# Performance work log

Measured on AMD Instinct MI355X. Metric: run time of the kernel, lower is better.

The kernel has to match this reference:

```python
import jax, jax.numpy as jnp
import numpy as np

DIM = 384
HEADS = 12
HD = DIM // HEADS  # 32
WIN = 16
N = WIN * WIN      # 256
B = 256            # num_windows * batch
K = 5              # dwc kernel size
EPS = 1e-6


def setup_inputs() -> dict:
    key = jax.random.key(0)
    ks = jax.random.split(key, 8)
    u = lambda k, shape, fan_in: jax.random.uniform(
        k, shape, jnp.float32, -1.0 / np.sqrt(fan_in), 1.0 / np.sqrt(fan_in))
    return {
        "x": jax.random.normal(ks[0], (B, N, DIM), jnp.float32),
        # nn.Linear(dim, 3*dim): weight [3C, C], bias [3C]
        "qkv_w": u(ks[1], (3 * DIM, DIM), DIM),
        "qkv_b": u(ks[2], (3 * DIM,), DIM),
        # nn.Parameter initialized to zeros
        "pos_enc": jnp.zeros((1, N, DIM), jnp.float32),
        # depthwise Conv2d(HD, HD, K, groups=HD): weight [HD, 1, K, K]
        "dwc_w": u(ks[3], (HD, 1, K, K), K * K),
        "dwc_b": u(ks[4], (HD,), K * K),
        "proj_w": u(ks[5], (DIM, DIM), DIM),
        "proj_b": u(ks[6], (DIM,), DIM),
    }


def reference(x, qkv_w, qkv_b, pos_enc, dwc_w, dwc_b, proj_w, proj_b):
    Bsz, Nn, C = x.shape
    qkv = x @ qkv_w.T + qkv_b                     # [B, N, 3C]
    q, k, v = jnp.split(qkv, 3, axis=-1)          # each [B, N, C]
    k = k + pos_enc
    q = jax.nn.relu(q)
    k = jax.nn.relu(k)

    def to_heads(t):  # 'b n (h c) -> (b h) n c'
        return t.reshape(Bsz, Nn, HEADS, HD).transpose(0, 2, 1, 3).reshape(Bsz * HEADS, Nn, HD)

    q, k, v = to_heads(q), to_heads(k), to_heads(v)
    # explicit fp32 (autocast disabled block in original)
    qf = q.astype(jnp.float32)
    kf = k.astype(jnp.float32)
    vf = v.astype(jnp.float32)

    z = 1.0 / (jnp.einsum('bic,bc->bi', qf, kf.sum(axis=1)) + EPS)  # [BH, N]

    i = j = Nn
    c = d = HD
    if i * j * (c + d) > c * d * (i + j):  # kv-first (true for N=256, HD=32)
        kv = jnp.einsum('bjc,bjd->bcd', kf, vf)            # [BH, c, d]
        out = jnp.einsum('bic,bcd,bi->bid', qf, kv, z)     # [BH, N, d]
    else:
        qk = jnp.einsum('bic,bjc->bij', qf, kf)
        out = jnp.einsum('bij,bjd,bi->bid', qk, vf, z)

    # depthwise conv on v: 'b (w h) c -> b c w h'
    num = int(Nn ** 0.5)
    fm = vf.reshape(Bsz * HEADS, num, num, HD).transpose(0, 3, 1, 2)  # NCHW
    fm = jax.lax.conv_general_dilated(
        fm, dwc_w, window_strides=(1, 1),
        padding=[(K // 2, K // 2), (K // 2, K // 2)],
        dimension_numbers=('NCHW', 'OIHW', 'NCHW'),
        feature_group_count=HD)
    fm = fm + dwc_b[None, :, None, None]
    fm = fm.transpose(0, 2, 3, 1).reshape(Bsz * HEADS, Nn, HD)  # 'b c w h -> b (w h) c'

    out = out + fm
    # '(b h) n c -> b n (h c)'
    out = out.reshape(Bsz, HEADS, Nn, HD).transpose(0, 2, 1, 3).reshape(Bsz, Nn, C)
    return out @ proj_w.T + proj_b
```

## Files before the change

kernel.cpp:

```cpp
#include <hip/hip_runtime.h>
#include <stdint.h>
#include <stddef.h>


typedef _Float16 f16;
typedef __attribute__((ext_vector_type(4))) _Float16 f16x4;
typedef __attribute__((ext_vector_type(8))) _Float16 f16x8;
typedef __attribute__((ext_vector_type(4))) float floatx4;

#define DEV __device__ __forceinline__

DEV void async16(const void* g, void* l) {
  __builtin_amdgcn_global_load_lds(
      (const __attribute__((address_space(1))) void*)g,
      (__attribute__((address_space(3))) void*)l,
      16, 0, 0);
}

DEV floatx4 mfma16(f16x8 a, f16x8 b, floatx4 c) {
  return __builtin_amdgcn_mfma_f32_16x16x32_f16(a, b, c, 0, 0, 0);
}

DEV f16x4 cvt4(float4 v) {
  f16x4 h;
  h[0] = (f16)v.x; h[1] = (f16)v.y; h[2] = (f16)v.z; h[3] = (f16)v.w;
  return h;
}

__global__ __launch_bounds__(256) void cvt_kernel(
    const float* __restrict__ src, f16* __restrict__ dst, int n4) {
  const int stride = gridDim.x * 256;
  for (int i = blockIdx.x * 256 + threadIdx.x; i < n4; i += stride) {
    float4 v = ((const float4*)src)[i];
    ((f16x4*)dst)[i] = cvt4(v);
  }
}

__global__ __launch_bounds__(256) void qkv_kernel(
    const f16* __restrict__ A, const f16* __restrict__ W,
    const float* __restrict__ bias, const float* __restrict__ pos,
    f16* __restrict__ q_ws, f16* __restrict__ kT_ws, f16* __restrict__ vT_ws) {
  __shared__ __align__(16) f16 Af[2][128 * 64];
  __shared__ __align__(16) f16 Wf[2][128 * 64];
  const int tid = threadIdx.x;
  const int lane = tid & 63, wave = tid >> 6;
  const int quad = lane >> 4, lr = lane & 15;
  const int wm = wave >> 1, wn = wave & 1;
  const int bx = blockIdx.x;
  const int ga = bx / 72, rem = bx - ga * 72;
  const int nblk = rem >> 3, gc = rem & 7;
  const int m0 = (ga * 8 + gc) * 128, n0 = nblk * 128;
  const int rl = lane >> 3;
  const int lcol = (lane & 7) ^ rl;

  floatx4 acc[4][4] = {};

  const f16* ap[4];
  const f16* wp[4];
#pragma unroll
  for (int t2 = 0; t2 < 4; ++t2) {
    const int row = (wave * 4 + t2) * 8 + rl;
    ap[t2] = A + (size_t)(m0 + row) * 384 + lcol * 8;
    wp[t2] = W + (size_t)(n0 + row) * 384 + lcol * 8;
  }

#pragma unroll
  for (int t2 = 0; t2 < 4; ++t2) {
    const int ch = wave * 4 + t2;
    async16(ap[t2], (char*)Af[0] + ch * 1024);
    async16(wp[t2], (char*)Wf[0] + ch * 1024);
  }
  __syncthreads();

#pragma unroll
  for (int kt = 0; kt < 6; ++kt) {
    const int p = kt & 1;
    if (kt < 5) {
#pragma unroll
      for (int t2 = 0; t2 < 4; ++t2) {
        const int ch = wave * 4 + t2;
        async16(ap[t2] + (kt + 1) * 64, (char*)Af[p ^ 1] + ch * 1024);
        async16(wp[t2] + (kt + 1) * 64, (char*)Wf[p ^ 1] + ch * 1024);
      }
    }
#pragma unroll
    for (int s = 0; s < 2; ++s) {
      const int pc = ((quad + s * 4) ^ (lr & 7)) * 16;
      f16x8 af[4], wf[4];
#pragma unroll
      for (int mt = 0; mt < 4; ++mt)
        af[mt] = *(const f16x8*)((const char*)Af[p] +
                                 (wm * 64 + mt * 16 + lr) * 128 + pc);
#pragma unroll
      for (int nt = 0; nt < 4; ++nt)
        wf[nt] = *(const f16x8*)((const char*)Wf[p] +
                                 (wn * 64 + nt * 16 + lr) * 128 + pc);
#pragma unroll
      for (int mt = 0; mt < 4; ++mt)
#pragma unroll
        for (int nt = 0; nt < 4; ++nt)
          acc[mt][nt] = mfma16(af[mt], wf[nt], acc[mt][nt]);
    }
    __syncthreads();
  }

  float bv[4];
#pragma unroll
  for (int nt = 0; nt < 4; ++nt)
    bv[nt] = bias[n0 + wn * 64 + nt * 16 + lr];

  const int cls = nblk / 3;
  const int cbase = (nblk - cls * 3) * 128;
  if (cls == 0) {
#pragma unroll
    for (int mt = 0; mt < 4; ++mt) {
#pragma unroll
      for (int r = 0; r < 4; ++r) {
        const int m = m0 + wm * 64 + mt * 16 + quad * 4 + r;
        const int bwin = m >> 8, t = m & 255;
#pragma unroll
        for (int nt = 0; nt < 4; ++nt) {
          const int c = cbase + wn * 64 + nt * 16 + lr;
          const int h = c >> 5, hd = c & 31;
          const float val = fmaxf(acc[mt][nt][r] + bv[nt], 0.f);
          q_ws[(size_t)(bwin * 12 + h) * 8192 + t * 32 + hd] = (f16)val;
        }
      }
    }
  } else {
#pragma unroll
    for (int mt = 0; mt < 4; ++mt) {
      const int mb = m0 + wm * 64 + mt * 16 + quad * 4;
      const int bwin = mb >> 8, t0 = mb & 255;
#pragma unroll
      for (int nt = 0; nt < 4; ++nt) {
        const int c = cbase + wn * 64 + nt * 16 + lr;
        const int h = c >> 5, hd = c & 31;
        f16x4 pk;
        if (cls == 1) {
#pragma unroll
          for (int r = 0; r < 4; ++r)
            pk[r] = (f16)fmaxf(acc[mt][nt][r] + bv[nt] + pos[(t0 + r) * 384 + c], 0.f);
          *(f16x4*)(kT_ws + (size_t)(bwin * 12 + h) * 8192 + hd * 256 + t0) = pk;
        } else {
#pragma unroll
          for (int r = 0; r < 4; ++r)
            pk[r] = (f16)(acc[mt][nt][r] + bv[nt]);
          *(f16x4*)(vT_ws + (size_t)(bwin * 12 + h) * 8192 + hd * 256 + t0) = pk;
        }
      }
    }
  }
}

__global__ __launch_bounds__(256) void attn_kernel(
    const f16* __restrict__ q_ws, const f16* __restrict__ kT_ws,
    const f16* __restrict__ vT_ws, const float* __restrict__ dwc_w,
    const float* __restrict__ dwc_b, f16* __restrict__ y_ws) {
  __shared__ __align__(16) char khb[16640];
  __shared__ __align__(16) char vhb[16640];
  __shared__ float psum[8 * 32];
  __shared__ float ksum[4][32];
  __shared__ float zbuf[256];
  __shared__ __align__(16) f16 kvT[32 * 40];

  const int tid = threadIdx.x;
  const int lane = tid & 63, wave = tid >> 6;
  const int quad = lane >> 4, lr = lane & 15;
  const size_t base = (size_t)blockIdx.x * 8192;

#pragma unroll
  for (int t2 = 0; t2 < 4; ++t2) {
    const int is = wave * 4 + t2;
    async16(kT_ws + base + is * 512 + lane * 8, khb + is * 1040);
    async16(vT_ws + base + is * 512 + lane * 8, vhb + is * 1040);
  }
  __syncthreads();

  {
    const int c = tid & 31, seg = tid >> 5;
    const char* kr = khb + (c >> 1) * 1040 + (c & 1) * 512;
    float s = 0.f;
#pragma unroll
    for (int j8 = 0; j8 < 32; j8 += 8) {
      f16x8 a = *(const f16x8*)(kr + (seg * 32 + j8) * 2);
#pragma unroll
      for (int j = 0; j < 8; ++j) s += (float)a[j];
    }
    psum[seg * 32 + c] = s;
  }
  {
    const int m2 = wave & 1, n2 = wave >> 1;
    const int ck = m2 * 16 + lr, cv = n2 * 16 + lr;
    const char* krow = khb + (ck >> 1) * 1040 + (ck & 1) * 512;
    const char* vrow = vhb + (cv >> 1) * 1040 + (cv & 1) * 512;
    floatx4 kacc = {};
#pragma unroll
    for (int s = 0; s < 8; ++s) {
      f16x8 ka = *(const f16x8*)(krow + (s * 32 + quad * 8) * 2);
      f16x8 vb = *(const f16x8*)(vrow + (s * 32 + quad * 8) * 2);
      kacc = mfma16(ka, vb, kacc);
    }
    f16x4 kk;
#pragma unroll
    for (int r = 0; r < 4; ++r) kk[r] = (f16)kacc[r];
    *(f16x4*)(kvT + (n2 * 16 + lr) * 40 + m2 * 16 + quad * 4) = kk;
  }
  __syncthreads();

  if (lane < 32) {
    float s = 0.f;
#pragma unroll
    for (int seg = 0; seg < 8; ++seg) s += psum[seg * 32 + lane];
    ksum[wave][lane] = s;
  }

  {
    uint32_t* fmu = (uint32_t*)khb;
    const int cg = lr, xr = wave * 4 + quad, c0 = cg * 2;
    float a0[16], a1[16];
    const float b0v = dwc_b[c0], b1v = dwc_b[c0 + 1];
#pragma unroll
    for (int yy = 0; yy < 16; ++yy) { a0[yy] = b0v; a1[yy] = b1v; }
    const char* v0 = vhb + cg * 1040;
#pragma unroll
    for (int dx = 0; dx < 5; ++dx) {
      const int xx = xr + dx - 2;
      if (xx < 0 || xx > 15) continue;
      float r0[16], r1[16];
      f16x8 h0 = *(const f16x8*)(v0 + xx * 32);
      f16x8 h1 = *(const f16x8*)(v0 + xx * 32 + 16);
      f16x8 h2 = *(const f16x8*)(v0 + 512 + xx * 32);
      f16x8 h3 = *(const f16x8*)(v0 + 512 + xx * 32 + 16);
#pragma unroll
      for (int j = 0; j < 8; ++j) {
        r0[j] = (float)h0[j]; r0[8 + j] = (float)h1[j];
        r1[j] = (float)h2[j]; r1[8 + j] = (float)h3[j];
      }
#pragma unroll
      for (int dy = 0; dy < 5; ++dy) {
        const float w0 = dwc_w[c0 * 25 + dx * 5 + dy];
        const float w1 = dwc_w[(c0 + 1) * 25 + dx * 5 + dy];
#pragma unroll
        for (int yy = 0; yy < 16; ++yy) {
          const int ys = yy + dy - 2;
          if (ys >= 0 && ys < 16) {
            a0[yy] += w0 * r0[ys];
            a1[yy] += w1 * r1[ys];
          }
        }
      }
    }
#pragma unroll
    for (int yy = 0; yy < 16; ++yy) {
      const uint32_t lo = (uint32_t)__builtin_bit_cast(uint16_t, (f16)a0[yy]);
      const uint32_t hi = (uint32_t)__builtin_bit_cast(uint16_t, (f16)a1[yy]);
      fmu[(xr * 16 + yy) * 16 + cg] = lo | (hi << 16);
    }
  }

  {
    f16x8 qa[4], kb[2];
#pragma unroll
    for (int mm = 0; mm < 4; ++mm)
      qa[mm] = *(const f16x8*)(q_ws + base +
                               (size_t)(wave * 64 + mm * 16 + lr) * 32 + quad * 8);

    float ksv[8];
#pragma unroll
    for (int j = 0; j < 8; ++j) ksv[j] = ksum[wave][quad * 8 + j];
#pragma unroll
    for (int mm = 0; mm < 4; ++mm) {
      float dot = 0.f;
#pragma unroll
      for (int j = 0; j < 8; ++j) dot += (float)qa[mm][j] * ksv[j];
      dot += __shfl_xor(dot, 16);
      dot += __shfl_xor(dot, 32);
      if (quad == 0) zbuf[wave * 64 + mm * 16 + lr] = 1.f / (dot + 1e-6f);
    }

    floatx4 oacc[4][2] = {};
#pragma unroll
    for (int nt = 0; nt < 2; ++nt)
      kb[nt] = *(const f16x8*)(kvT + (nt * 16 + lr) * 40 + quad * 8);
#pragma unroll
    for (int mm = 0; mm < 4; ++mm)
#pragma unroll
      for (int nt = 0; nt < 2; ++nt)
        oacc[mm][nt] = mfma16(qa[mm], kb[nt], oacc[mm][nt]);

    const f16* fmb = (const f16*)khb;
#pragma unroll
    for (int mm = 0; mm < 4; ++mm) {
#pragma unroll
      for (int r = 0; r < 4; ++r) {
        const int i = wave * 64 + mm * 16 + quad * 4 + r;
        const float zi = zbuf[i];
#pragma unroll
        for (int nt = 0; nt < 2; ++nt) {
          const int d = nt * 16 + lr;
          const float val = oacc[mm][nt][r] * zi + (float)fmb[i * 32 + d];
          y_ws[base + (size_t)i * 32 + d] = (f16)val;
        }
      }
    }
  }
}

__global__ __launch_bounds__(256) void proj_kernel(
    const f16* __restrict__ Y, const f16* __restrict__ Wh,
    const float* __restrict__ bias, float* __restrict__ out) {
  __shared__ __align__(16) f16 Af[2][128 * 64];
  __shared__ __align__(16) f16 Wf[2][128 * 64];
  const int tid = threadIdx.x;
  const int lane = tid & 63, wave = tid >> 6;
  const int quad = lane >> 4, lr = lane & 15;
  const int wm = wave >> 1, wn = wave & 1;
  const int bx = blockIdx.x;
  const int ga = bx / 24, rem = bx - ga * 24;
  const int nblk = rem >> 3, gc = rem & 7;
  const int m0 = (ga * 8 + gc) * 128, n0 = nblk * 128;
  const int bwin = m0 >> 8, tbase = m0 & 255;
  const int rl = lane >> 3;
  const int lcol = (lane & 7) ^ rl;

  floatx4 acc[4][4] = {};

  const f16* ap[4];
  const f16* wp[4];
#pragma unroll
  for (int t2 = 0; t2 < 4; ++t2) {
    const int rowl = (wave * 4 + t2) * 8 + rl;
    ap[t2] = Y + (size_t)(bwin * 12 + (lcol >> 2)) * 8192 +
             (size_t)(tbase + rowl) * 32 + (lcol & 3) * 8;
    wp[t2] = Wh + (size_t)(n0 + rowl) * 384 + lcol * 8;
  }

#pragma unroll
  for (int t2 = 0; t2 < 4; ++t2) {
    const int ch = wave * 4 + t2;
    async16(ap[t2], (char*)Af[0] + ch * 1024);
    async16(wp[t2], (char*)Wf[0] + ch * 1024);
  }
  __syncthreads();

#pragma unroll
  for (int kt = 0; kt < 6; ++kt) {
    const int p = kt & 1;
    if (kt < 5) {
#pragma unroll
      for (int t2 = 0; t2 < 4; ++t2) {
        const int ch = wave * 4 + t2;
        async16(ap[t2] + (size_t)(kt + 1) * 16384, (char*)Af[p ^ 1] + ch * 1024);
        async16(wp[t2] + (kt + 1) * 64, (char*)Wf[p ^ 1] + ch * 1024);
      }
    }
#pragma unroll
    for (int s = 0; s < 2; ++s) {
      const int pc = ((quad + s * 4) ^ (lr & 7)) * 16;
      f16x8 af[4], wf[4];
#pragma unroll
      for (int mt = 0; mt < 4; ++mt)
        af[mt] = *(const f16x8*)((const char*)Af[p] +
                                 (wm * 64 + mt * 16 + lr) * 128 + pc);
#pragma unroll
      for (int nt = 0; nt < 4; ++nt)
        wf[nt] = *(const f16x8*)((const char*)Wf[p] +
                                 (wn * 64 + nt * 16 + lr) * 128 + pc);
#pragma unroll
      for (int mt = 0; mt < 4; ++mt)
#pragma unroll
        for (int nt = 0; nt < 4; ++nt)
          acc[mt][nt] = mfma16(af[mt], wf[nt], acc[mt][nt]);
    }
    __syncthreads();
  }

  float bv[4];
#pragma unroll
  for (int nt = 0; nt < 4; ++nt)
    bv[nt] = bias[n0 + wn * 64 + nt * 16 + lr];
#pragma unroll
  for (int mt = 0; mt < 4; ++mt)
#pragma unroll
    for (int r = 0; r < 4; ++r) {
      const int m = m0 + wm * 64 + mt * 16 + quad * 4 + r;
#pragma unroll
      for (int nt = 0; nt < 4; ++nt) {
        const int n = n0 + wn * 64 + nt * 16 + lr;
        out[(size_t)m * 384 + n] = acc[mt][nt][r] + bv[nt];
      }
    }
}

extern "C" void kernel_launch(void* const* d_in, const int* in_sizes, int n_in,
                              void* d_out, int out_size, void* d_ws, size_t ws_size,
                              hipStream_t stream) {
  const float* x = (const float*)d_in[0];
  const float* qkv_w = (const float*)d_in[1];
  const float* qkv_b = (const float*)d_in[2];
  const float* pos = (const float*)d_in[3];
  const float* dwc_w = (const float*)d_in[4];
  const float* dwc_b = (const float*)d_in[5];
  const float* proj_w = (const float*)d_in[6];
  const float* proj_b = (const float*)d_in[7];
  float* out = (float*)d_out;

  const size_t WS_NEEDED = 150994944;
  if (ws_size < WS_NEEDED) return;

  char* ws = (char*)d_ws;
  f16* q_ws = (f16*)(ws);
  f16* kT_ws = (f16*)(ws + 50331648);
  f16* vT_ws = (f16*)(ws + 100663296);

  f16* xh = (f16*)d_out;
  f16* qwh = (f16*)((char*)d_out + 50331648);
  f16* pwh = (f16*)(ws + 50331648);

  cvt_kernel<<<2048, 256, 0, stream>>>(x, xh, 6291456);
  cvt_kernel<<<432, 256, 0, stream>>>(qkv_w, qwh, 110592);
  qkv_kernel<<<4608, 256, 0, stream>>>(xh, qwh, qkv_b, pos,
                                       q_ws, kT_ws, vT_ws);
  attn_kernel<<<3072, 256, 0, stream>>>(q_ws, kT_ws, vT_ws,
                                        dwc_w, dwc_b, q_ws );
  cvt_kernel<<<144, 256, 0, stream>>>(proj_w, pwh, 36864);
  proj_kernel<<<1536, 256, 0, stream>>>(q_ws, pwh, proj_b, out);
}
```

Measured before the change: 359.7 us.

## Single-buffer QKV GEMM tiles, stage Q epilogue through LDS, prefetch Q early

The QKV GEMM drops LDS double buffering and instead syncs, loads, and computes each k-tile in turn, halving the shared memory it uses. The freed LDS then holds the Q output tile in a swizzled layout, so q_ws is written as contiguous 16-byte vectors instead of scattered 2-byte stores. The attention kernel issues its Q fragment loads before the barrier so they overlap the async K/V loads. The cost is that global-to-LDS transfers no longer overlap with MFMA work inside the GEMM, though higher occupancy may partly hide this.

```diff
diff --git a/kernel.cpp b/kernel.cpp
--- a/kernel.cpp
+++ b/kernel.cpp
@@ -40,8 +40,8 @@
     const f16* __restrict__ A, const f16* __restrict__ W,
     const float* __restrict__ bias, const float* __restrict__ pos,
     f16* __restrict__ q_ws, f16* __restrict__ kT_ws, f16* __restrict__ vT_ws) {
-  __shared__ __align__(16) f16 Af[2][128 * 64];
-  __shared__ __align__(16) f16 Wf[2][128 * 64];
+  __shared__ __align__(16) f16 Af[128 * 64];
+  __shared__ __align__(16) f16 Wf[128 * 64];
   const int tid = threadIdx.x;
   const int lane = tid & 63, wave = tid >> 6;
   const int quad = lane >> 4, lr = lane & 15;
@@ -64,36 +64,26 @@
     wp[t2] = W + (size_t)(n0 + row) * 384 + lcol * 8;
   }
 
-#pragma unroll
-  for (int t2 = 0; t2 < 4; ++t2) {
-    const int ch = wave * 4 + t2;
-    async16(ap[t2], (char*)Af[0] + ch * 1024);
-    async16(wp[t2], (char*)Wf[0] + ch * 1024);
-  }
-  __syncthreads();
-
-#pragma unroll
   for (int kt = 0; kt < 6; ++kt) {
-    const int p = kt & 1;
-    if (kt < 5) {
-#pragma unroll
-      for (int t2 = 0; t2 < 4; ++t2) {
-        const int ch = wave * 4 + t2;
-        async16(ap[t2] + (kt + 1) * 64, (char*)Af[p ^ 1] + ch * 1024);
-        async16(wp[t2] + (kt + 1) * 64, (char*)Wf[p ^ 1] + ch * 1024);
-      }
-    }
+    __syncthreads();
+#pragma unroll
+    for (int t2 = 0; t2 < 4; ++t2) {
+      const int ch = wave * 4 + t2;
+      async16(ap[t2] + kt * 64, (char*)Af + ch * 1024);
+      async16(wp[t2] + kt * 64, (char*)Wf + ch * 1024);
+    }
+    __syncthreads();
 #pragma unroll
     for (int s = 0; s < 2; ++s) {
       const int pc = ((quad + s * 4) ^ (lr & 7)) * 16;
       f16x8 af[4], wf[4];
 #pragma unroll
       for (int mt = 0; mt < 4; ++mt)
-        af[mt] = *(const f16x8*)((const char*)Af[p] +
+        af[mt] = *(const f16x8*)((const char*)Af +
                                  (wm * 64 + mt * 16 + lr) * 128 + pc);
 #pragma unroll
       for (int nt = 0; nt < 4; ++nt)
-        wf[nt] = *(const f16x8*)((const char*)Wf[p] +
+        wf[nt] = *(const f16x8*)((const char*)Wf +
                                  (wn * 64 + nt * 16 + lr) * 128 + pc);
 #pragma unroll
       for (int mt = 0; mt < 4; ++mt)
@@ -101,7 +91,6 @@
         for (int nt = 0; nt < 4; ++nt)
           acc[mt][nt] = mfma16(af[mt], wf[nt], acc[mt][nt]);
     }
-    __syncthreads();
   }
 
   float bv[4];
@@ -112,20 +101,38 @@
   const int cls = nblk / 3;
   const int cbase = (nblk - cls * 3) * 128;
   if (cls == 0) {
+    __syncthreads();
+    f16* buf = wn ? Wf : Af;
 #pragma unroll
     for (int mt = 0; mt < 4; ++mt) {
 #pragma unroll
-      for (int r = 0; r < 4; ++r) {
-        const int m = m0 + wm * 64 + mt * 16 + quad * 4 + r;
-        const int bwin = m >> 8, t = m & 255;
-#pragma unroll
-        for (int nt = 0; nt < 4; ++nt) {
-          const int c = cbase + wn * 64 + nt * 16 + lr;
-          const int h = c >> 5, hd = c & 31;
+      for (int nt = 0; nt < 4; ++nt) {
+#pragma unroll
+        for (int r = 0; r < 4; ++r) {
+          const int row = wm * 64 + mt * 16 + quad * 4 + r;
+          const int cb = ((nt * 16 + lr) * 2) ^ (((row >> 2) & 7) << 4);
           const float val = fmaxf(acc[mt][nt][r] + bv[nt], 0.f);
-          q_ws[(size_t)(bwin * 12 + h) * 8192 + t * 32 + hd] = (f16)val;
+          *(f16*)((char*)buf + row * 128 + cb) = (f16)val;
         }
       }
+    }
+    __syncthreads();
+    const int t = tid >> 1;
+    const int tg = (m0 & 255) + t;
+    const int bwin = m0 >> 8;
+    const int hbase = nblk * 4;
+    const int sw = ((t >> 2) & 7) << 4;
+    const char* arow = (const char*)Af + t * 128;
+    const char* wrow = (const char*)Wf + t * 128;
+#pragma unroll
+    for (int hh = 0; hh < 2; ++hh) {
+      const int h = (tid & 1) * 2 + hh;
+      const char* src = (h & 2) ? wrow : arow;
+      const int off0 = (h & 1) * 64;
+      f16* dst = q_ws + (size_t)(bwin * 12 + hbase + h) * 8192 + tg * 32;
+#pragma unroll
+      for (int s = 0; s < 4; ++s)
+        *(f16x8*)(dst + s * 8) = *(const f16x8*)(src + ((off0 + s * 16) ^ sw));
     }
   } else {
 #pragma unroll
@@ -175,6 +182,11 @@
     async16(kT_ws + base + is * 512 + lane * 8, khb + is * 1040);
     async16(vT_ws + base + is * 512 + lane * 8, vhb + is * 1040);
   }
+  f16x8 qa[4];
+#pragma unroll
+  for (int mm = 0; mm < 4; ++mm)
+    qa[mm] = *(const f16x8*)(q_ws + base +
+                             (size_t)(wave * 64 + mm * 16 + lr) * 32 + quad * 8);
   __syncthreads();
 
   {
@@ -260,12 +272,6 @@
   }
 
   {
-    f16x8 qa[4], kb[2];
-#pragma unroll
-    for (int mm = 0; mm < 4; ++mm)
-      qa[mm] = *(const f16x8*)(q_ws + base +
-                               (size_t)(wave * 64 + mm * 16 + lr) * 32 + quad * 8);
-
     float ksv[8];
 #pragma unroll
     for (int j = 0; j < 8; ++j) ksv[j] = ksum[wave][quad * 8 + j];
@@ -280,6 +286,7 @@
     }
 
     floatx4 oacc[4][2] = {};
+    f16x8 kb[2];
 #pragma unroll
     for (int nt = 0; nt < 2; ++nt)
       kb[nt] = *(const f16x8*)(kvT + (nt * 16 + lr) * 40 + quad * 8);
```

Result: no change. 360.8 us (+0.3%).
